# Optimization experiments

Hardware: AMD Instinct MI355X
Metric: run time of the kernel (lower is better)

Reference implementation:

```python
import jax, jax.numpy as jnp
import numpy as np

SEQ_LEN, BATCH, VOCAB, EMB, HID, LAYERS = 128, 128, 10000, 512, 512, 2

def setup_inputs() -> dict:
    key = jax.random.key(0)
    ks = jax.random.split(key, 8)
    k = float(np.sqrt(1.0 / HID))
    inputs = jax.random.randint(ks[0], (SEQ_LEN, BATCH), 0, VOCAB)
    hidden = jnp.zeros((LAYERS, BATCH, HID), dtype=jnp.float32)
    emb = jax.random.uniform(ks[1], (VOCAB, EMB), jnp.float32, -0.1, 0.1)
    W0 = jax.random.uniform(ks[2], (HID, EMB + HID), jnp.float32, -k, k)
    b0 = jax.random.uniform(ks[3], (HID,), jnp.float32, -k, k)
    W1 = jax.random.uniform(ks[4], (HID, 2 * HID), jnp.float32, -k, k)
    b1 = jax.random.uniform(ks[5], (HID,), jnp.float32, -k, k)
    Wout = jax.random.uniform(ks[6], (VOCAB, HID), jnp.float32, -0.1, 0.1)
    bout = jnp.zeros((VOCAB,), dtype=jnp.float32)
    return {"inputs": inputs, "hidden": hidden, "emb": emb, "W0": W0, "b0": b0,
            "W1": W1, "b1": b1, "Wout": Wout, "bout": bout}

def reference(inputs, hidden, emb, W0, b0, W1, b1, Wout, bout):
    # inputs: [S,B] int; hidden: [L,B,H]
    def step(h, tok):
        x = emb[tok]                                              # [B,E]
        h0 = jnp.tanh(jnp.concatenate([x, h[0]], axis=1) @ W0.T + b0)   # [B,H]
        h1 = jnp.tanh(jnp.concatenate([h0, h[1]], axis=1) @ W1.T + b1)  # [B,H]
        logits_t = h1 @ Wout.T + bout                             # [B,V]
        return jnp.stack([h0, h1]), logits_t
    hidden_final, logits = jax.lax.scan(step, hidden, inputs)
    return logits, hidden_final
```

## Files before the change

### kernel.cpp

```cpp
#include <hip/hip_runtime.h>
#include <hip/hip_fp16.h>

typedef _Float16 f16;
typedef _Float16 f16x4 __attribute__((ext_vector_type(4)));
typedef _Float16 f16x8 __attribute__((ext_vector_type(8)));
typedef float f32x4 __attribute__((ext_vector_type(4)));
typedef unsigned u32x4 __attribute__((ext_vector_type(4)));

#define S_LEN 128
#define B_SZ  128
#define VOC   10000
#define VPAD  10240
#define HIDN  512
#define NBLK  64
#define NFLAG (NBLK * 4)

#define VMCNT(n) do { asm volatile("s_waitcnt vmcnt(" #n ")" ::: "memory"); \
                      __builtin_amdgcn_sched_barrier(0); } while (0)

__device__ __forceinline__ void gload_lds16(const void* g, void* l) {
  __builtin_amdgcn_global_load_lds(
      (const __attribute__((address_space(1))) void*)g,
      (__attribute__((address_space(3))) void*)l, 16, 0, 0);
}

__device__ __forceinline__ f16x8 ld16_dev(const f16* p) {
  u32x4 r;
  asm volatile("global_load_dwordx4 %0, %1, off sc1" : "=v"(r) : "v"(p));
  return __builtin_bit_cast(f16x8, r);
}
__device__ __forceinline__ void cstore8(f16* p, f16x4 v) {
  unsigned long long u = __builtin_bit_cast(unsigned long long, v);
  __hip_atomic_store((unsigned long long*)p, u, __ATOMIC_RELAXED, __HIP_MEMORY_SCOPE_AGENT);
}
__device__ __forceinline__ void stflag_dev(unsigned* p, unsigned v) {
  asm volatile("global_store_dword %0, %1, off sc1" :: "v"(p), "v"(v) : "memory");
}

__device__ __forceinline__ float fast_tanh(float x) {
  float cx = fminf(8.f, fmaxf(-8.f, x));
  float e = __expf(2.f * cx);
  float d = e + 1.f, r;
  asm("v_rcp_f32 %0, %1" : "=v"(r) : "v"(d));
  return (e - 1.f) * r;
}

__global__ void convert_pad(const float* __restrict__ src, f16* __restrict__ dst,
                            int rows, int src_stride, int total) {
  int idx = blockIdx.x * 256 + threadIdx.x;
  if (idx >= total) return;
  int r = idx >> 9, c = idx & 511;
  float v = (r < rows) ? src[(size_t)r * src_stride + c] : 0.f;
  dst[idx] = (f16)v;
}

#define STAGE64(ktile) do {                                                   \
    _Pragma("unroll")                                                         \
    for (int it_ = 0; it_ < 4; ++it_) {                                       \
      int c_   = it_ * 256 + tid;                       \
      int row_ = c_ >> 3, sp_ = c_ & 7;                                       \
      int sl_  = sp_ ^ (row_ & 7);                    \
      gload_lds16(A + (size_t)(m0 + row_) * 512 + (ktile) * 64 + sl_ * 8,     \
                  &Asw[(size_t)(it_ * 256 + w * 64) * 8]);                    \
      gload_lds16(B + (size_t)(n0 + row_) * 512 + (ktile) * 64 + sl_ * 8,     \
                  &Bsw[(size_t)(it_ * 256 + w * 64) * 8]);                    \
    }                                                                         \
  } while (0)

template <typename CT>
__global__ __launch_bounds__(256) void gemm_k512(
    const f16* __restrict__ A, const f16* __restrict__ B,
    CT* __restrict__ C, const float* __restrict__ bias,
    int M, int N, int ldc)
{
  __shared__ f16 Asw[128 * 64];
  __shared__ f16 Bsw[128 * 64];
  const int tid  = threadIdx.x;
  const int lane = tid & 63, w = tid >> 6;
  const int wrow = w >> 1, wcol = w & 1;
  int nwg  = gridDim.x * gridDim.y;
  int orig = blockIdx.y * gridDim.x + blockIdx.x;
  int cpx  = nwg >> 3;
  int swz  = (orig & 7) * cpx + (orig >> 3);
  const int m0 = (swz / gridDim.x) * 128, n0 = (swz % gridDim.x) * 128;
  const int rsel = lane & 15, ksl = lane >> 4;

  f32x4 acc[4][4] = {};

  for (int ktile = 0; ktile < 8; ++ktile) {
    __syncthreads();
    STAGE64(ktile);
    __syncthreads();
#pragma unroll
    for (int kt2 = 0; kt2 < 2; ++kt2) {
      f16x8 af[4], bf[4];
#pragma unroll
      for (int i = 0; i < 4; ++i) {
        int ar = wrow * 64 + i * 16 + rsel;
        af[i] = *(const f16x8*)&Asw[ar * 64 + (((kt2 * 4 + ksl) ^ (ar & 7)) * 8)];
        int br = wcol * 64 + i * 16 + rsel;
        bf[i] = *(const f16x8*)&Bsw[br * 64 + (((kt2 * 4 + ksl) ^ (br & 7)) * 8)];
      }
#pragma unroll
      for (int i = 0; i < 4; ++i)
#pragma unroll
        for (int j = 0; j < 4; ++j)
          acc[i][j] = __builtin_amdgcn_mfma_f32_16x16x32_f16(bf[j], af[i], acc[i][j], 0, 0, 0);
    }
  }

#pragma unroll
  for (int i = 0; i < 4; ++i) {
    int row = m0 + wrow * 64 + i * 16 + rsel;
    if (row >= M) continue;
#pragma unroll
    for (int j = 0; j < 4; ++j) {
      int nb = n0 + wcol * 64 + j * 16 + ksl * 4;
      if (nb >= N) continue;
      f32x4 v = acc[i][j];
      if (bias) {
        f32x4 bv = *(const f32x4*)(bias + nb);
        v += bv;
      }
      if constexpr (__is_same(CT, float)) {
        *(f32x4*)&C[(size_t)row * ldc + nb] = v;
      } else {
        f16x4 hv;
#pragma unroll
        for (int q = 0; q < 4; ++q) hv[q] = (f16)v[q];
        *(f16x4*)&C[(size_t)row * ldc + nb] = hv;
      }
    }
  }
}

__global__ __launch_bounds__(256, 1) void rnn_recur(
    const int* __restrict__ tok,
    const float* __restrict__ W0,
    const float* __restrict__ W1,
    const float* __restrict__ b1,
    const f16* __restrict__ P0h,
    f16* __restrict__ h0ring,
    const f16* __restrict__ h1init,
    f16* __restrict__ H1,
    float* __restrict__ outHid,
    unsigned* __restrict__ flags)
{
  __shared__ f16 wlds[3][16 * 512];
  const int tid = threadIdx.x;
  const int lane = tid & 63, w = tid >> 6;
  const int cgI = blockIdx.x & 31, bg = blockIdx.x >> 5;
  const int col0 = cgI * 16;
  const int rowstart = bg * 64 + w * 16;
  const int rsel = lane & 15, ksl = lane >> 4;
  const int fidx = blockIdx.x * 4 + w;

  for (int it = tid; it < 3 * 16 * 64; it += 256) {
    int s = it >> 10;
    int rem = it & 1023;
    int c = rem >> 6, ks = rem & 63;
    int n = col0 + c;
    const float* srcp;
    if (s == 0)      srcp = W0 + (size_t)n * 1024 + 512 + ks * 8;
    else if (s == 1) srcp = W1 + (size_t)n * 1024 + ks * 8;
    else             srcp = W1 + (size_t)n * 1024 + 512 + ks * 8;
    f16x8 v;
#pragma unroll
    for (int j = 0; j < 8; ++j) v[j] = (f16)srcp[j];
    *(f16x8*)&wlds[s][c * 512 + ((ks ^ (c & 7)) * 8)] = v;
  }
  const f32x4 b1q = *(const f32x4*)(b1 + col0 + ksl * 4);
  __syncthreads();

  const int myrow = rowstart + rsel;
  const size_t hrow = (size_t)myrow * HIDN;
  const int colq = col0 + ksl * 4;
  const unsigned* fptr = flags + 4 * lane;

  f16x8 hf[16];
  f32x4 part1;

  for (int p = 0; p <= S_LEN + 1; ++p) {
    const bool doH0 = (p <= S_LEN - 1);
    const bool doH1 = (p >= 2);

    if (doH1) {
      f32x4 t = b1q;
#pragma unroll
      for (int kt = 0; kt < 16; ++kt) {
        int ks = kt * 4 + ksl;
        f16x8 b = *(const f16x8*)&wlds[1][rsel * 512 + ((ks ^ (rsel & 7)) * 8)];
        t = __builtin_amdgcn_mfma_f32_16x16x32_f16(b, hf[kt], t, 0, 0, 0);
      }
      part1 = t;
    }
    float pa0, pa1, pa2, pa3;
    if (doH0) {
      int t_ = tok[p * B_SZ + myrow];
      f16x4 pv = *(const f16x4*)&P0h[(size_t)t_ * HIDN + colq];
      pa0 = (float)pv[0]; pa1 = (float)pv[1]; pa2 = (float)pv[2]; pa3 = (float)pv[3];
      asm volatile("" : "+v"(pa0), "+v"(pa1), "+v"(pa2), "+v"(pa3));
    }

    if (p >= 1) {
      const unsigned tgt = (unsigned)p;
      for (;;) {
        u32x4 f;
        asm volatile("global_load_dwordx4 %0, %1, off sc1\n\ts_waitcnt vmcnt(0)"
                     : "=v"(f) : "v"(fptr) : "memory");
        int ok = (f[0] >= tgt) & (f[1] >= tgt) & (f[2] >= tgt) & (f[3] >= tgt);
        if (__all(ok)) break;
      }
    }

    if (p <= S_LEN) {
      const f16* src = h0ring + (size_t)((p - 1) & 3) * B_SZ * HIDN;
#pragma unroll
      for (int kt = 0; kt < 16; ++kt)
        hf[kt] = ld16_dev(src + hrow + kt * 32 + ksl * 8);
    }
    f16x8 h1f[16];
    if (doH1) {
      const f16* h1src = (p == 2) ? h1init : H1 + (size_t)(p - 3) * B_SZ * HIDN;
#pragma unroll
      for (int kt = 0; kt < 16; ++kt)
        h1f[kt] = ld16_dev(h1src + hrow + kt * 32 + ksl * 8);
    }

    float v0, v1, v2, v3;
    if (doH0) {
      if (doH1) { VMCNT(16); } else { VMCNT(0); }
      f32x4 acc0 = {pa0, pa1, pa2, pa3};
#pragma unroll
      for (int kt = 0; kt < 16; ++kt) {
        int ks = kt * 4 + ksl;
        f16x8 b = *(const f16x8*)&wlds[0][rsel * 512 + ((ks ^ (rsel & 7)) * 8)];
        acc0 = __builtin_amdgcn_mfma_f32_16x16x32_f16(b, hf[kt], acc0, 0, 0, 0);
      }
      v0 = fast_tanh(acc0[0]); v1 = fast_tanh(acc0[1]);
      v2 = fast_tanh(acc0[2]); v3 = fast_tanh(acc0[3]);
      f16* dst = h0ring + (size_t)(p & 3) * B_SZ * HIDN;
      f16x4 hv = {(f16)v0, (f16)v1, (f16)v2, (f16)v3};
      cstore8(&dst[hrow + colq], hv);
    }
    if (doH1) {
      if (doH0) { VMCNT(1); } else { VMCNT(0); }
      f32x4 acc1 = part1;
#pragma unroll
      for (int kt = 0; kt < 16; ++kt) {
        int ks = kt * 4 + ksl;
        f16x8 b = *(const f16x8*)&wlds[2][rsel * 512 + ((ks ^ (rsel & 7)) * 8)];
        acc1 = __builtin_amdgcn_mfma_f32_16x16x32_f16(b, h1f[kt], acc1, 0, 0, 0);
      }
      float u0 = fast_tanh(acc1[0]), u1 = fast_tanh(acc1[1]);
      float u2 = fast_tanh(acc1[2]), u3 = fast_tanh(acc1[3]);
      f16* h1dst = H1 + (size_t)(p - 2) * B_SZ * HIDN;
      f16x4 hv = {(f16)u0, (f16)u1, (f16)u2, (f16)u3};
      cstore8(&h1dst[hrow + colq], hv);
      if (p == S_LEN + 1) {
        f32x4 fv = {u0, u1, u2, u3};
        *(f32x4*)&outHid[(size_t)(B_SZ * HIDN) + hrow + colq] = fv;
      }
    }
    if (doH0 && p == S_LEN - 1) {
      f32x4 fv = {v0, v1, v2, v3};
      *(f32x4*)&outHid[hrow + colq] = fv;
    }

    if (p <= S_LEN) {
      VMCNT(0);
      if (lane == 0) stflag_dev((unsigned*)flags + fidx, (unsigned)(p + 1));
    }
  }
}

extern "C" void kernel_launch(void* const* d_in, const int* in_sizes, int n_in,
                              void* d_out, int out_size, void* d_ws, size_t ws_size,
                              hipStream_t stream) {
  (void)in_sizes; (void)n_in; (void)out_size; (void)ws_size;
  const int*   tok    = (const int*)d_in[0];
  const float* hidden = (const float*)d_in[1];
  const float* emb    = (const float*)d_in[2];
  const float* W0     = (const float*)d_in[3];
  const float* b0     = (const float*)d_in[4];
  const float* W1     = (const float*)d_in[5];
  const float* b1     = (const float*)d_in[6];
  const float* Wout   = (const float*)d_in[7];
  const float* bout   = (const float*)d_in[8];

  char* ws = (char*)d_ws;
  size_t off = 0;
  f16* embf16  = (f16*)(ws + off); off += (size_t)VPAD * 512 * 2;
  f16* woutf16 = (f16*)(ws + off); off += (size_t)VPAD * 512 * 2;
  f16* w0xf16  = (f16*)(ws + off); off += (size_t)512 * 512 * 2;
  f16* P0h     = (f16*)(ws + off); off += (size_t)VOC * 512 * 2;
  f16* H1      = (f16*)(ws + off); off += (size_t)S_LEN * B_SZ * 512 * 2;
  f16* h0ring  = (f16*)(ws + off); off += (size_t)4 * B_SZ * 512 * 2;
  f16* h1init  = (f16*)(ws + off); off += (size_t)B_SZ * 512 * 2;
  unsigned* flags = (unsigned*)(ws + off); off += NFLAG * 4;

  float* outHid = (float*)d_out + (size_t)S_LEN * B_SZ * VOC;

  hipMemsetAsync(flags, 0, NFLAG * 4, stream);

  int tot = VPAD * 512;
  convert_pad<<<(tot + 255) / 256, 256, 0, stream>>>(emb,  embf16,  VOC, 512, tot);
  convert_pad<<<(tot + 255) / 256, 256, 0, stream>>>(Wout, woutf16, VOC, 512, tot);
  tot = 512 * 512;
  convert_pad<<<(tot + 255) / 256, 256, 0, stream>>>(W0, w0xf16, 512, 1024, tot);
  tot = B_SZ * 512;
  convert_pad<<<(tot + 255) / 256, 256, 0, stream>>>(hidden, h0ring + (size_t)3 * B_SZ * 512, B_SZ, 512, tot);
  convert_pad<<<(tot + 255) / 256, 256, 0, stream>>>(hidden + (size_t)B_SZ * 512, h1init, B_SZ, 512, tot);

  gemm_k512<f16><<<dim3(4, VPAD / 128), 256, 0, stream>>>(
      embf16, w0xf16, P0h, b0, VOC, 512, 512);

  {
    void* args[] = {(void*)&tok, (void*)&W0, (void*)&W1, (void*)&b1, (void*)&P0h,
                    (void*)&h0ring, (void*)&h1init, (void*)&H1, (void*)&outHid, (void*)&flags};
    hipLaunchCooperativeKernel((const void*)rnn_recur, dim3(NBLK), dim3(256), args, 0, stream);
  }

  gemm_k512<float><<<dim3(79, 128), 256, 0, stream>>>(
      H1, woutf16, (float*)d_out, bout, S_LEN * B_SZ, VOC, VOC);
}
```

Measured before the change: 1.208 ms.

## Scope recurrence flags per batch group and double-buffer GEMM LDS staging

The recurrent kernel now waits only on the 128 flags belonging to its own batch-row group (32 column blocks × 4 waves), not on all 256 flags across both groups. Each lane polls two flags instead of four, which should cut cross-group stalls and polling traffic. Separately, the K=512 GEMM gains double-buffered LDS staging so the next k-tile's global loads overlap the MFMA compute on the current one. The GEMM change doubles shared memory per block, which may lower occupancy.

```diff
diff --git a/kernel.cpp b/kernel.cpp
--- a/kernel.cpp
+++ b/kernel.cpp
@@ -5,6 +5,7 @@
 typedef _Float16 f16x4 __attribute__((ext_vector_type(4)));
 typedef _Float16 f16x8 __attribute__((ext_vector_type(8)));
 typedef float f32x4 __attribute__((ext_vector_type(4)));
+typedef unsigned u32x2 __attribute__((ext_vector_type(2)));
 typedef unsigned u32x4 __attribute__((ext_vector_type(4)));
 
 #define S_LEN 128
@@ -13,7 +14,7 @@
 #define VPAD  10240
 #define HIDN  512
 #define NBLK  64
-#define NFLAG (NBLK * 4)
+#define NFLAG 256
 
 #define VMCNT(n) do { asm volatile("s_waitcnt vmcnt(" #n ")" ::: "memory"); \
                       __builtin_amdgcn_sched_barrier(0); } while (0)
@@ -54,16 +55,35 @@
   dst[idx] = (f16)v;
 }
 
-#define STAGE64(ktile) do {                                                   \
+#define STAGE64(ktile, bufv) do {                                             \
     _Pragma("unroll")                                                         \
     for (int it_ = 0; it_ < 4; ++it_) {                                       \
       int c_   = it_ * 256 + tid;                       \
       int row_ = c_ >> 3, sp_ = c_ & 7;                                       \
       int sl_  = sp_ ^ (row_ & 7);                    \
       gload_lds16(A + (size_t)(m0 + row_) * 512 + (ktile) * 64 + sl_ * 8,     \
-                  &Asw[(size_t)(it_ * 256 + w * 64) * 8]);                    \
+                  &Asw[bufv][(size_t)(it_ * 256 + w * 64) * 8]);              \
       gload_lds16(B + (size_t)(n0 + row_) * 512 + (ktile) * 64 + sl_ * 8,     \
-                  &Bsw[(size_t)(it_ * 256 + w * 64) * 8]);                    \
+                  &Bsw[bufv][(size_t)(it_ * 256 + w * 64) * 8]);              \
+    }                                                                         \
+  } while (0)
+
+#define COMPUTE64(bufv) do {                                                  \
+    _Pragma("unroll")                                                         \
+    for (int kt2 = 0; kt2 < 2; ++kt2) {                                       \
+      f16x8 af[4], bf[4];                                                     \
+      _Pragma("unroll")                                                       \
+      for (int i = 0; i < 4; ++i) {                                           \
+        int ar = wrow * 64 + i * 16 + rsel;                                   \
+        af[i] = *(const f16x8*)&Asw[bufv][ar * 64 + (((kt2 * 4 + ksl) ^ (ar & 7)) * 8)]; \
+        int br = wcol * 64 + i * 16 + rsel;                                   \
+        bf[i] = *(const f16x8*)&Bsw[bufv][br * 64 + (((kt2 * 4 + ksl) ^ (br & 7)) * 8)]; \
+      }                                                                       \
+      _Pragma("unroll")                                                       \
+      for (int i = 0; i < 4; ++i)                                             \
+        _Pragma("unroll")                                                     \
+        for (int j = 0; j < 4; ++j)                                           \
+          acc[i][j] = __builtin_amdgcn_mfma_f32_16x16x32_f16(bf[j], af[i], acc[i][j], 0, 0, 0); \
     }                                                                         \
   } while (0)
 
@@ -73,8 +93,8 @@
     CT* __restrict__ C, const float* __restrict__ bias,
     int M, int N, int ldc)
 {
-  __shared__ f16 Asw[128 * 64];
-  __shared__ f16 Bsw[128 * 64];
+  __shared__ f16 Asw[2][128 * 64];
+  __shared__ f16 Bsw[2][128 * 64];
   const int tid  = threadIdx.x;
   const int lane = tid & 63, w = tid >> 6;
   const int wrow = w >> 1, wcol = w & 1;
@@ -87,26 +107,15 @@
 
   f32x4 acc[4][4] = {};
 
-  for (int ktile = 0; ktile < 8; ++ktile) {
+  STAGE64(0, 0);
+  __syncthreads();
+  for (int kt = 0; kt < 8; kt += 2) {
+    if (kt + 1 < 8) STAGE64(kt + 1, 1);
+    COMPUTE64(0);
     __syncthreads();
-    STAGE64(ktile);
+    if (kt + 2 < 8) STAGE64(kt + 2, 0);
+    COMPUTE64(1);
     __syncthreads();
-#pragma unroll
-    for (int kt2 = 0; kt2 < 2; ++kt2) {
-      f16x8 af[4], bf[4];
-#pragma unroll
-      for (int i = 0; i < 4; ++i) {
-        int ar = wrow * 64 + i * 16 + rsel;
-        af[i] = *(const f16x8*)&Asw[ar * 64 + (((kt2 * 4 + ksl) ^ (ar & 7)) * 8)];
-        int br = wcol * 64 + i * 16 + rsel;
-        bf[i] = *(const f16x8*)&Bsw[br * 64 + (((kt2 * 4 + ksl) ^ (br & 7)) * 8)];
-      }
-#pragma unroll
-      for (int i = 0; i < 4; ++i)
-#pragma unroll
-        for (int j = 0; j < 4; ++j)
-          acc[i][j] = __builtin_amdgcn_mfma_f32_16x16x32_f16(bf[j], af[i], acc[i][j], 0, 0, 0);
-    }
   }
 
 #pragma unroll
@@ -153,7 +162,8 @@
   const int col0 = cgI * 16;
   const int rowstart = bg * 64 + w * 16;
   const int rsel = lane & 15, ksl = lane >> 4;
-  const int fidx = blockIdx.x * 4 + w;
+  unsigned* gflags = flags + bg * 128;
+  const int fidx = cgI * 4 + w;
 
   for (int it = tid; it < 3 * 16 * 64; it += 256) {
     int s = it >> 10;
@@ -175,7 +185,7 @@
   const int myrow = rowstart + rsel;
   const size_t hrow = (size_t)myrow * HIDN;
   const int colq = col0 + ksl * 4;
-  const unsigned* fptr = flags + 4 * lane;
+  const unsigned* fptr = gflags + 2 * lane;
 
   f16x8 hf[16];
   f32x4 part1;
@@ -205,10 +215,10 @@
     if (p >= 1) {
       const unsigned tgt = (unsigned)p;
       for (;;) {
-        u32x4 f;
-        asm volatile("global_load_dwordx4 %0, %1, off sc1\n\ts_waitcnt vmcnt(0)"
+        u32x2 f;
+        asm volatile("global_load_dwordx2 %0, %1, off sc1\n\ts_waitcnt vmcnt(0)"
                      : "=v"(f) : "v"(fptr) : "memory");
-        int ok = (f[0] >= tgt) & (f[1] >= tgt) & (f[2] >= tgt) & (f[3] >= tgt);
+        int ok = (f[0] >= tgt) & (f[1] >= tgt);
         if (__all(ok)) break;
       }
     }
@@ -269,7 +279,7 @@
 
     if (p <= S_LEN) {
       VMCNT(0);
-      if (lane == 0) stflag_dev((unsigned*)flags + fidx, (unsigned)(p + 1));
+      if (lane == 0) stflag_dev(gflags + fidx, (unsigned)(p + 1));
     }
   }
 }
```

New measurement: 1.202 ms. No clear change (-0.5%).
